# Kernel tuning notes

Hardware: AMD Instinct MI355X
Metric: run time of the kernel (lower is better)

Reference implementation:

```python
import jax, jax.numpy as jnp
import numpy as np

N, E, H, G, T = 10000, 160000, 256, 64, 1


def _lin(k, cin, cout):
    return jax.random.normal(k, (cin, cout), jnp.float32) * np.float32(1.0 / np.sqrt(cin))


def setup_inputs() -> dict:
    key = jax.random.key(0)
    ks = jax.random.split(key, 12)
    d = {}
    i = 0
    for p in ("lp", "pk", "lg"):
        d[p + "_node_feats"] = jax.random.normal(ks[i], (N, H), jnp.float32); i += 1
        d[p + "_edge_feats"] = jax.random.normal(ks[i], (E, H), jnp.float32); i += 1
        d[p + "_edge_index"] = jax.random.randint(ks[i], (2, E), 0, N); i += 1
        d[p + "_batch"] = jnp.sort(jax.random.randint(ks[i], (N,), 0, G)); i += 1
    wk = jax.random.split(jax.random.fold_in(key, 1), 6)
    d["W1"] = _lin(wk[0], H, H); d["b1"] = jnp.zeros((H,), jnp.float32)
    d["W2"] = _lin(wk[1], H, H); d["b2"] = jnp.zeros((H,), jnp.float32)
    d["W3"] = _lin(wk[2], H, H); d["b3"] = jnp.zeros((H,), jnp.float32)
    d["V1"] = _lin(wk[3], 2 * H, H); d["c1"] = jnp.zeros((H,), jnp.float32)
    d["V2"] = _lin(wk[4], H, H); d["c2"] = jnp.zeros((H,), jnp.float32)
    d["V3"] = _lin(wk[5], H, T); d["c3"] = jnp.zeros((T,), jnp.float32)
    d["num_graphs"] = G
    return d


def _mlp1(x, W1, b1, W2, b2, W3, b3):
    # make_mlp(c_in=H, c_hidden=H, c_out=H, num_layers=2), SiLU activations,
    # mlp_output_activation=SiLU
    h = jax.nn.silu(x @ W1 + b1)
    h = jax.nn.silu(h @ W2 + b2)
    return jax.nn.silu(h @ W3 + b3)


def _mlp2(x, V1, c1, V2, c2, V3, c3):
    # make_mlp(c_in=2H, c_hidden=H, c_out=num_tasks), output_activation=None
    h = jax.nn.silu(x @ V1 + c1)
    h = jax.nn.silu(h @ V2 + c2)
    return h @ V3 + c3


def _head(nf, ef, eidx, batch, num_graphs, p1, p2):
    n = nf.shape[0]
    # nodes branch: MLP then scatter-sum to graph level
    pooled_n = jax.ops.segment_sum(_mlp1(nf, *p1), batch, num_segments=num_graphs)
    # edges branch: MLP, scatter-sum edges->receiver nodes, then nodes->graphs
    pe = jax.ops.segment_sum(_mlp1(ef, *p1), eidx[1], num_segments=n)
    pooled_e = jax.ops.segment_sum(pe, batch, num_segments=num_graphs)
    return _mlp2(jnp.concatenate([pooled_n, pooled_e], axis=-1), *p2)


def reference(lp_node_feats, lp_edge_feats, lp_edge_index, lp_batch,
              pk_node_feats, pk_edge_feats, pk_edge_index, pk_batch,
              lg_node_feats, lg_edge_feats, lg_edge_index, lg_batch,
              num_graphs, W1, b1, W2, b2, W3, b3, V1, c1, V2, c2, V3, c3):
    p1 = (W1, b1, W2, b2, W3, b3)
    p2 = (V1, c1, V2, c2, V3, c3)
    out_lp = _head(lp_node_feats, lp_edge_feats, lp_edge_index, lp_batch, num_graphs, p1, p2)
    out_pk = _head(pk_node_feats, pk_edge_feats, pk_edge_index, pk_batch, num_graphs, p1, p2)
    out_lg = _head(lg_node_feats, lg_edge_feats, lg_edge_index, lg_batch, num_graphs, p1, p2)
    # output = pooled['ligand_pocket'] - pooled['pocket'] - pooled['ligand']
    return out_lp - out_pk - out_lg
```

## Files before the change

kernel.cpp:

```cpp
#include <hip/hip_runtime.h>
#include <hip/hip_bf16.h>

#define HD 256
#define NG 64
#define NNODES 10000
#define NEDGES 160000
#define MBLK 256
#define NTHREADS 512

typedef __attribute__((ext_vector_type(8))) short short8;
typedef __attribute__((ext_vector_type(4))) float f32x4;

__device__ __forceinline__ unsigned short f2bf(float f) {
  unsigned int u = __float_as_uint(f);
  u += 0x7FFFu + ((u >> 16) & 1u);
  return (unsigned short)(u >> 16);
}
__device__ __forceinline__ float silu_f(float x) {
  return x / (1.0f + __expf(-x));
}

__global__ void prep_weights(const float* __restrict__ W1, const float* __restrict__ W2,
                             const float* __restrict__ W3, unsigned short* __restrict__ Wt) {
  int idx = blockIdx.x * blockDim.x + threadIdx.x;
  int mat = idx >> 16;
  int rem = idx & 65535;
  int n = rem >> 8, k = rem & 255;
  const float* W = (mat == 0) ? W1 : (mat == 1) ? W2 : W3;
  Wt[idx] = f2bf(W[k * 256 + n]);
}

__global__ __launch_bounds__(NTHREADS, 2)
void fused_mlp1_pool(
    const float* __restrict__ nf0, const float* __restrict__ ef0,
    const int* __restrict__ ei0, const int* __restrict__ bt0,
    const float* __restrict__ nf1, const float* __restrict__ ef1,
    const int* __restrict__ ei1, const int* __restrict__ bt1,
    const float* __restrict__ nf2, const float* __restrict__ ef2,
    const int* __restrict__ ei2, const int* __restrict__ bt2,
    const float* __restrict__ b1, const float* __restrict__ b2,
    const float* __restrict__ b3,
    const unsigned short* __restrict__ Wt, float* __restrict__ pooled) {

  extern __shared__ char lds_raw[];
  char* stageB = lds_raw;
  char* SB = lds_raw + 131072;

  const int tid = threadIdx.x;
  const int wid = tid >> 6, lane = tid & 63;
  const int l15 = lane & 15, lhi = lane >> 4;
  const int wr = wid >> 2, wc = wid & 3;

  const int bid = blockIdx.x;
  const int head = bid / 85;
  const int r85 = bid % 85;
  const int isEdge = (r85 >= 5) ? 1 : 0;
  const int lb = isEdge ? (r85 - 5) : r85;
  const int Bs = isEdge ? 80 : 5;
  const int rows = isEdge ? NEDGES : NNODES;
  const int ntiles = (rows + MBLK - 1) / MBLK;

  const float* X; const int* bt; const int* recv;
  if (head == 0)      { X = isEdge ? ef0 : nf0; bt = bt0; recv = ei0 + NEDGES; }
  else if (head == 1) { X = isEdge ? ef1 : nf1; bt = bt1; recv = ei1 + NEDGES; }
  else                { X = isEdge ? ef2 : nf2; bt = bt2; recv = ei2 + NEDGES; }
  float* pool = pooled + (head * 2 + isEdge) * (NG * HD);

  f32x4 pacc[4][2];
  #pragma unroll
  for (int mt = 0; mt < 4; mt++)
    #pragma unroll
    for (int n = 0; n < 2; n++) pacc[mt][n] = (f32x4){0.f, 0.f, 0.f, 0.f};

  #pragma unroll
  for (int i = 0; i < 4; i++) ((int4*)SB)[tid + NTHREADS * i] = make_int4(0, 0, 0, 0);
  __syncthreads();

  for (int t = lb; t < ntiles; t += Bs) {
    const int rbase = t * MBLK;

    #pragma unroll 4
    for (int i = 0; i < 32; i++) {
      int rr = wid + i * 8;
      int gr = rbase + rr; if (gr > rows - 1) gr = rows - 1;
      f32x4 v = *(const f32x4*)(X + (long)gr * HD + lane * 4);
      unsigned long long pk =
          (unsigned long long)f2bf(v.x) |
          ((unsigned long long)f2bf(v.y) << 16) |
          ((unsigned long long)f2bf(v.z) << 32) |
          ((unsigned long long)f2bf(v.w) << 48);
      int byte = (rr * 512 + lane * 8) ^ ((rr & 7) << 4);
      *(unsigned long long*)(stageB + byte) = pk;
    }
    if (tid < MBLK) {
      int gr = rbase + tid;
      if (gr < rows) {
        int g = isEdge ? bt[recv[gr]] : bt[gr];
        int byte = (g * 512 + tid * 2) ^ ((g & 7) << 4);
        *(unsigned short*)(SB + byte) = 0x3F80;
      }
    }
    __syncthreads();

    #pragma unroll 1
    for (int layer = 0; layer < 3; layer++) {
      const unsigned short* Wl = Wt + layer * 65536;
      const float* bias = (layer == 0) ? b1 : (layer == 1) ? b2 : b3;

      f32x4 acc[8][4];
      #pragma unroll
      for (int n = 0; n < 4; n++) {
        float bv = bias[wc * 64 + n * 16 + l15];
        #pragma unroll
        for (int m = 0; m < 8; m++) acc[m][n] = (f32x4){bv, bv, bv, bv};
      }

      #pragma unroll 2
      for (int k = 0; k < 8; k++) {
        short8 bfrag[4];
        #pragma unroll
        for (int n = 0; n < 4; n++) {
          int cout = wc * 64 + n * 16 + l15;
          bfrag[n] = *(const short8*)(Wl + cout * 256 + k * 32 + lhi * 8);
        }
        #pragma unroll
        for (int m = 0; m < 8; m++) {
          int row = wr * 128 + m * 16 + l15;
          int byte = (row * 512 + k * 64 + lhi * 16) ^ ((row & 7) << 4);
          short8 a = *(const short8*)(stageB + byte);
          #pragma unroll
          for (int n = 0; n < 4; n++)
            acc[m][n] = __builtin_amdgcn_mfma_f32_16x16x32_bf16(a, bfrag[n], acc[m][n], 0, 0, 0);
        }
      }
      __syncthreads();

      if (layer < 2) {
        #pragma unroll
        for (int m = 0; m < 8; m++) {
          #pragma unroll
          for (int n = 0; n < 4; n++) {
            int col = wc * 64 + n * 16 + l15;
            #pragma unroll
            for (int j = 0; j < 4; j++) {
              int row = wr * 128 + m * 16 + lhi * 4 + j;
              unsigned short hv = f2bf(silu_f(acc[m][n][j]));
              int byte = (row * 512 + col * 2) ^ ((row & 7) << 4);
              *(unsigned short*)(stageB + byte) = hv;
            }
          }
        }
      } else {
        #pragma unroll
        for (int m = 0; m < 8; m++) {
          #pragma unroll
          for (int n = 0; n < 4; n++) {
            int col = wc * 64 + n * 16 + l15;
            int row0 = wr * 128 + m * 16 + lhi * 4;
            unsigned long long pk =
                (unsigned long long)f2bf(silu_f(acc[m][n][0])) |
                ((unsigned long long)f2bf(silu_f(acc[m][n][1])) << 16) |
                ((unsigned long long)f2bf(silu_f(acc[m][n][2])) << 32) |
                ((unsigned long long)f2bf(silu_f(acc[m][n][3])) << 48);
            int byte = (col * 512 + row0 * 2) ^ ((col & 7) << 4);
            *(unsigned long long*)(stageB + byte) = pk;
          }
        }
      }
      __syncthreads();
    }

    #pragma unroll 2
    for (int k = 0; k < 8; k++) {
      short8 bh[2];
      #pragma unroll
      for (int n = 0; n < 2; n++) {
        int col = wid * 32 + n * 16 + l15;
        int byte = (col * 512 + k * 64 + lhi * 16) ^ ((col & 7) << 4);
        bh[n] = *(const short8*)(stageB + byte);
      }
      #pragma unroll
      for (int mt = 0; mt < 4; mt++) {
        int g = mt * 16 + l15;
        int byte = (g * 512 + k * 64 + lhi * 16) ^ ((g & 7) << 4);
        short8 aS = *(const short8*)(SB + byte);
        #pragma unroll
        for (int n = 0; n < 2; n++)
          pacc[mt][n] = __builtin_amdgcn_mfma_f32_16x16x32_bf16(aS, bh[n], pacc[mt][n], 0, 0, 0);
      }
    }
    __syncthreads();
    #pragma unroll
    for (int i = 0; i < 4; i++) ((int4*)SB)[tid + NTHREADS * i] = make_int4(0, 0, 0, 0);
    __syncthreads();
  }

  #pragma unroll
  for (int mt = 0; mt < 4; mt++) {
    #pragma unroll
    for (int n = 0; n < 2; n++) {
      int col = wid * 32 + n * 16 + l15;
      #pragma unroll
      for (int j = 0; j < 4; j++) {
        int g = mt * 16 + lhi * 4 + j;
        unsafeAtomicAdd(&pool[g * HD + col], pacc[mt][n][j]);
      }
    }
  }
}

__global__ void mlp2_kernel(const float* __restrict__ pooled,
                            const float* __restrict__ V1, const float* __restrict__ c1,
                            const float* __restrict__ V2, const float* __restrict__ c2,
                            const float* __restrict__ V3, const float* __restrict__ c3,
                            float* __restrict__ out) {
  __shared__ float x[512];
  __shared__ float hb[256];
  __shared__ float wsum[4];
  const int g = blockIdx.x, t = threadIdx.x;
  float total = 0.0f;

  #pragma unroll 1
  for (int head = 0; head < 3; head++) {
    x[t]       = pooled[(head * 2 + 0) * NG * HD + g * HD + t];
    x[t + 256] = pooled[(head * 2 + 1) * NG * HD + g * HD + t];
    __syncthreads();

    float a = c1[t];
    #pragma unroll 8
    for (int k = 0; k < 512; k++) a += x[k] * V1[k * HD + t];
    a = silu_f(a);
    hb[t] = a;
    __syncthreads();

    float b = c2[t];
    #pragma unroll 8
    for (int k = 0; k < 256; k++) b += hb[k] * V2[k * HD + t];
    b = silu_f(b);

    float p = b * V3[t];
    #pragma unroll
    for (int off = 32; off > 0; off >>= 1) p += __shfl_down(p, off, 64);
    if ((t & 63) == 0) wsum[t >> 6] = p;
    __syncthreads();
    if (t == 0) {
      float s = wsum[0] + wsum[1] + wsum[2] + wsum[3] + c3[0];
      total += (head == 0) ? s : -s;
    }
    __syncthreads();
  }
  if (t == 0) out[g] = total;
}

extern "C" void kernel_launch(void* const* d_in, const int* in_sizes, int n_in,
                              void* d_out, int out_size, void* d_ws, size_t ws_size,
                              hipStream_t stream) {
  const float* nf0 = (const float*)d_in[0];
  const float* ef0 = (const float*)d_in[1];
  const int*   ei0 = (const int*)d_in[2];
  const int*   bt0 = (const int*)d_in[3];
  const float* nf1 = (const float*)d_in[4];
  const float* ef1 = (const float*)d_in[5];
  const int*   ei1 = (const int*)d_in[6];
  const int*   bt1 = (const int*)d_in[7];
  const float* nf2 = (const float*)d_in[8];
  const float* ef2 = (const float*)d_in[9];
  const int*   ei2 = (const int*)d_in[10];
  const int*   bt2 = (const int*)d_in[11];
  const float* W1 = (const float*)d_in[12]; const float* b1 = (const float*)d_in[13];
  const float* W2 = (const float*)d_in[14]; const float* b2 = (const float*)d_in[15];
  const float* W3 = (const float*)d_in[16]; const float* b3 = (const float*)d_in[17];
  const float* V1 = (const float*)d_in[18]; const float* c1 = (const float*)d_in[19];
  const float* V2 = (const float*)d_in[20]; const float* c2 = (const float*)d_in[21];
  const float* V3 = (const float*)d_in[22]; const float* c3 = (const float*)d_in[23];

  float* pooled = (float*)d_ws;
  unsigned short* Wt = (unsigned short*)((char*)d_ws + 393216);

  hipMemsetAsync(pooled, 0, 393216, stream);
  prep_weights<<<768, 256, 0, stream>>>(W1, W2, W3, Wt);

  hipFuncSetAttribute((const void*)fused_mlp1_pool,
                      hipFuncAttributeMaxDynamicSharedMemorySize, 163840);
  fused_mlp1_pool<<<255, NTHREADS, 163840, stream>>>(
      nf0, ef0, ei0, bt0, nf1, ef1, ei1, bt1, nf2, ef2, ei2, bt2,
      b1, b2, b3, Wt, pooled);

  mlp2_kernel<<<64, 256, 0, stream>>>(pooled, V1, c1, V2, c2, V3, c3, (float*)d_out);
}
```

Measured before the change: 1.373 ms.

## Use 1024-thread blocks, transposed MFMA epilogue with packed bf16 stores, split mlp2 per head

```diff
diff --git a/kernel.cpp b/kernel.cpp
--- a/kernel.cpp
+++ b/kernel.cpp
@@ -6,18 +6,18 @@
 #define NNODES 10000
 #define NEDGES 160000
 #define MBLK 256
-#define NTHREADS 512
+#define NTHREADS 1024
 
 typedef __attribute__((ext_vector_type(8))) short short8;
 typedef __attribute__((ext_vector_type(4))) float f32x4;
 
-__device__ __forceinline__ unsigned short f2bf(float f) {
-  unsigned int u = __float_as_uint(f);
-  u += 0x7FFFu + ((u >> 16) & 1u);
-  return (unsigned short)(u >> 16);
+__device__ __forceinline__ unsigned int pkbf2(float a, float b) {
+  __hip_bfloat162 h = __float22bfloat162_rn(float2{a, b});
+  return *reinterpret_cast<unsigned int*>(&h);
 }
 __device__ __forceinline__ float silu_f(float x) {
-  return x / (1.0f + __expf(-x));
+  float e = __builtin_amdgcn_exp2f(-1.442695041f * x);
+  return x * __builtin_amdgcn_rcpf(1.0f + e);
 }
 
 __global__ void prep_weights(const float* __restrict__ W1, const float* __restrict__ W2,
@@ -27,10 +27,11 @@
   int rem = idx & 65535;
   int n = rem >> 8, k = rem & 255;
   const float* W = (mat == 0) ? W1 : (mat == 1) ? W2 : W3;
-  Wt[idx] = f2bf(W[k * 256 + n]);
-}
-
-__global__ __launch_bounds__(NTHREADS, 2)
+  __hip_bfloat16 h = __float2bfloat16(W[k * 256 + n]);
+  Wt[idx] = *reinterpret_cast<unsigned short*>(&h);
+}
+
+__global__ __launch_bounds__(NTHREADS)
 void fused_mlp1_pool(
     const float* __restrict__ nf0, const float* __restrict__ ef0,
     const int* __restrict__ ei0, const int* __restrict__ bt0,
@@ -50,6 +51,7 @@
   const int wid = tid >> 6, lane = tid & 63;
   const int l15 = lane & 15, lhi = lane >> 4;
   const int wr = wid >> 2, wc = wid & 3;
+  const int wrow = wr * 64, wcol = wc * 64;
 
   const int bid = blockIdx.x;
   const int head = bid / 85;
@@ -66,31 +68,25 @@
   else                { X = isEdge ? ef2 : nf2; bt = bt2; recv = ei2 + NEDGES; }
   float* pool = pooled + (head * 2 + isEdge) * (NG * HD);
 
-  f32x4 pacc[4][2];
-  #pragma unroll
-  for (int mt = 0; mt < 4; mt++)
-    #pragma unroll
-    for (int n = 0; n < 2; n++) pacc[mt][n] = (f32x4){0.f, 0.f, 0.f, 0.f};
-
-  #pragma unroll
-  for (int i = 0; i < 4; i++) ((int4*)SB)[tid + NTHREADS * i] = make_int4(0, 0, 0, 0);
+  f32x4 pacc[4];
+  #pragma unroll
+  for (int mt = 0; mt < 4; mt++) pacc[mt] = (f32x4){0.f, 0.f, 0.f, 0.f};
+
+  #pragma unroll
+  for (int i = 0; i < 2; i++) ((int4*)SB)[tid + NTHREADS * i] = make_int4(0, 0, 0, 0);
   __syncthreads();
 
   for (int t = lb; t < ntiles; t += Bs) {
     const int rbase = t * MBLK;
 
     #pragma unroll 4
-    for (int i = 0; i < 32; i++) {
-      int rr = wid + i * 8;
+    for (int i = 0; i < 16; i++) {
+      int rr = wid + i * 16;
       int gr = rbase + rr; if (gr > rows - 1) gr = rows - 1;
       f32x4 v = *(const f32x4*)(X + (long)gr * HD + lane * 4);
-      unsigned long long pk =
-          (unsigned long long)f2bf(v.x) |
-          ((unsigned long long)f2bf(v.y) << 16) |
-          ((unsigned long long)f2bf(v.z) << 32) |
-          ((unsigned long long)f2bf(v.w) << 48);
+      uint2 pk = make_uint2(pkbf2(v.x, v.y), pkbf2(v.z, v.w));
       int byte = (rr * 512 + lane * 8) ^ ((rr & 7) << 4);
-      *(unsigned long long*)(stageB + byte) = pk;
+      *(uint2*)(stageB + byte) = pk;
     }
     if (tid < MBLK) {
       int gr = rbase + tid;
@@ -107,63 +103,73 @@
       const unsigned short* Wl = Wt + layer * 65536;
       const float* bias = (layer == 0) ? b1 : (layer == 1) ? b2 : b3;
 
-      f32x4 acc[8][4];
-      #pragma unroll
-      for (int n = 0; n < 4; n++) {
-        float bv = bias[wc * 64 + n * 16 + l15];
-        #pragma unroll
-        for (int m = 0; m < 8; m++) acc[m][n] = (f32x4){bv, bv, bv, bv};
+      f32x4 acc[4][4];
+      if (layer < 2) {
+        #pragma unroll
+        for (int ct = 0; ct < 4; ct++) {
+          f32x4 bv = *(const f32x4*)(bias + wcol + ct * 16 + lhi * 4);
+          #pragma unroll
+          for (int rt = 0; rt < 4; rt++) acc[rt][ct] = bv;
+        }
+      } else {
+        #pragma unroll
+        for (int ct = 0; ct < 4; ct++) {
+          float bv = bias[wcol + ct * 16 + l15];
+          #pragma unroll
+          for (int rt = 0; rt < 4; rt++) acc[rt][ct] = (f32x4){bv, bv, bv, bv};
+        }
       }
 
       #pragma unroll 2
       for (int k = 0; k < 8; k++) {
-        short8 bfrag[4];
-        #pragma unroll
-        for (int n = 0; n < 4; n++) {
-          int cout = wc * 64 + n * 16 + l15;
-          bfrag[n] = *(const short8*)(Wl + cout * 256 + k * 32 + lhi * 8);
-        }
-        #pragma unroll
-        for (int m = 0; m < 8; m++) {
-          int row = wr * 128 + m * 16 + l15;
+        short8 wfrag[4];
+        #pragma unroll
+        for (int ct = 0; ct < 4; ct++)
+          wfrag[ct] = *(const short8*)(Wl + (wcol + ct * 16 + l15) * 256 + k * 32 + lhi * 8);
+        #pragma unroll
+        for (int rt = 0; rt < 4; rt++) {
+          int row = wrow + rt * 16 + l15;
           int byte = (row * 512 + k * 64 + lhi * 16) ^ ((row & 7) << 4);
-          short8 a = *(const short8*)(stageB + byte);
-          #pragma unroll
-          for (int n = 0; n < 4; n++)
-            acc[m][n] = __builtin_amdgcn_mfma_f32_16x16x32_bf16(a, bfrag[n], acc[m][n], 0, 0, 0);
+          short8 xf = *(const short8*)(stageB + byte);
+          if (layer < 2) {
+            #pragma unroll
+            for (int ct = 0; ct < 4; ct++)
+              acc[rt][ct] = __builtin_amdgcn_mfma_f32_16x16x32_bf16(wfrag[ct], xf, acc[rt][ct], 0, 0, 0);
+          } else {
+            #pragma unroll
+            for (int ct = 0; ct < 4; ct++)
+              acc[rt][ct] = __builtin_amdgcn_mfma_f32_16x16x32_bf16(xf, wfrag[ct], acc[rt][ct], 0, 0, 0);
+          }
         }
       }
       __syncthreads();
 
       if (layer < 2) {
         #pragma unroll
-        for (int m = 0; m < 8; m++) {
-          #pragma unroll
-          for (int n = 0; n < 4; n++) {
-            int col = wc * 64 + n * 16 + l15;
-            #pragma unroll
-            for (int j = 0; j < 4; j++) {
-              int row = wr * 128 + m * 16 + lhi * 4 + j;
-              unsigned short hv = f2bf(silu_f(acc[m][n][j]));
-              int byte = (row * 512 + col * 2) ^ ((row & 7) << 4);
-              *(unsigned short*)(stageB + byte) = hv;
-            }
+        for (int rt = 0; rt < 4; rt++) {
+          int row = wrow + rt * 16 + l15;
+          #pragma unroll
+          for (int ct = 0; ct < 4; ct++) {
+            int c0 = wcol + ct * 16 + lhi * 4;
+            f32x4 a = acc[rt][ct];
+            uint2 pk = make_uint2(pkbf2(silu_f(a.x), silu_f(a.y)),
+                                  pkbf2(silu_f(a.z), silu_f(a.w)));
+            int byte = (row * 512 + c0 * 2) ^ ((row & 7) << 4);
+            *(uint2*)(stageB + byte) = pk;
           }
         }
       } else {
         #pragma unroll
-        for (int m = 0; m < 8; m++) {
-          #pragma unroll
-          for (int n = 0; n < 4; n++) {
-            int col = wc * 64 + n * 16 + l15;
-            int row0 = wr * 128 + m * 16 + lhi * 4;
-            unsigned long long pk =
-                (unsigned long long)f2bf(silu_f(acc[m][n][0])) |
-                ((unsigned long long)f2bf(silu_f(acc[m][n][1])) << 16) |
-                ((unsigned long long)f2bf(silu_f(acc[m][n][2])) << 32) |
-                ((unsigned long long)f2bf(silu_f(acc[m][n][3])) << 48);
+        for (int rt = 0; rt < 4; rt++) {
+          int row0 = wrow + rt * 16 + lhi * 4;
+          #pragma unroll
+          for (int ct = 0; ct < 4; ct++) {
+            int col = wcol + ct * 16 + l15;
+            f32x4 a = acc[rt][ct];
+            uint2 pk = make_uint2(pkbf2(silu_f(a.x), silu_f(a.y)),
+                                  pkbf2(silu_f(a.z), silu_f(a.w)));
             int byte = (col * 512 + row0 * 2) ^ ((col & 7) << 4);
-            *(unsigned long long*)(stageB + byte) = pk;
+            *(uint2*)(stageB + byte) = pk;
           }
         }
       }
@@ -172,39 +178,30 @@
 
     #pragma unroll 2
     for (int k = 0; k < 8; k++) {
-      short8 bh[2];
-      #pragma unroll
-      for (int n = 0; n < 2; n++) {
-        int col = wid * 32 + n * 16 + l15;
-        int byte = (col * 512 + k * 64 + lhi * 16) ^ ((col & 7) << 4);
-        bh[n] = *(const short8*)(stageB + byte);
-      }
+      int col = wid * 16 + l15;
+      int byteB = (col * 512 + k * 64 + lhi * 16) ^ ((col & 7) << 4);
+      short8 bh = *(const short8*)(stageB + byteB);
       #pragma unroll
       for (int mt = 0; mt < 4; mt++) {
         int g = mt * 16 + l15;
-        int byte = (g * 512 + k * 64 + lhi * 16) ^ ((g & 7) << 4);
-        short8 aS = *(const short8*)(SB + byte);
-        #pragma unroll
-        for (int n = 0; n < 2; n++)
-          pacc[mt][n] = __builtin_amdgcn_mfma_f32_16x16x32_bf16(aS, bh[n], pacc[mt][n], 0, 0, 0);
+        int byteA = (g * 512 + k * 64 + lhi * 16) ^ ((g & 7) << 4);
+        short8 aS = *(const short8*)(SB + byteA);
+        pacc[mt] = __builtin_amdgcn_mfma_f32_16x16x32_bf16(aS, bh, pacc[mt], 0, 0, 0);
       }
     }
     __syncthreads();
     #pragma unroll
-    for (int i = 0; i < 4; i++) ((int4*)SB)[tid + NTHREADS * i] = make_int4(0, 0, 0, 0);
+    for (int i = 0; i < 2; i++) ((int4*)SB)[tid + NTHREADS * i] = make_int4(0, 0, 0, 0);
     __syncthreads();
   }
 
   #pragma unroll
   for (int mt = 0; mt < 4; mt++) {
+    int col = wid * 16 + l15;
     #pragma unroll
-    for (int n = 0; n < 2; n++) {
-      int col = wid * 32 + n * 16 + l15;
-      #pragma unroll
-      for (int j = 0; j < 4; j++) {
-        int g = mt * 16 + lhi * 4 + j;
-        unsafeAtomicAdd(&pool[g * HD + col], pacc[mt][n][j]);
-      }
+    for (int j = 0; j < 4; j++) {
+      int g = mt * 16 + lhi * 4 + j;
+      unsafeAtomicAdd(&pool[g * HD + col], pacc[mt][j]);
     }
   }
 }
@@ -217,39 +214,33 @@
   __shared__ float x[512];
   __shared__ float hb[256];
   __shared__ float wsum[4];
-  const int g = blockIdx.x, t = threadIdx.x;
-  float total = 0.0f;
-
-  #pragma unroll 1
-  for (int head = 0; head < 3; head++) {
-    x[t]       = pooled[(head * 2 + 0) * NG * HD + g * HD + t];
-    x[t + 256] = pooled[(head * 2 + 1) * NG * HD + g * HD + t];
-    __syncthreads();
-
-    float a = c1[t];
-    #pragma unroll 8
-    for (int k = 0; k < 512; k++) a += x[k] * V1[k * HD + t];
-    a = silu_f(a);
-    hb[t] = a;
-    __syncthreads();
-
-    float b = c2[t];
-    #pragma unroll 8
-    for (int k = 0; k < 256; k++) b += hb[k] * V2[k * HD + t];
-    b = silu_f(b);
-
-    float p = b * V3[t];
-    #pragma unroll
-    for (int off = 32; off > 0; off >>= 1) p += __shfl_down(p, off, 64);
-    if ((t & 63) == 0) wsum[t >> 6] = p;
-    __syncthreads();
-    if (t == 0) {
-      float s = wsum[0] + wsum[1] + wsum[2] + wsum[3] + c3[0];
-      total += (head == 0) ? s : -s;
-    }
-    __syncthreads();
+  const int g = blockIdx.x & 63, head = blockIdx.x >> 6, t = threadIdx.x;
+
+  x[t]       = pooled[(head * 2 + 0) * NG * HD + g * HD + t];
+  x[t + 256] = pooled[(head * 2 + 1) * NG * HD + g * HD + t];
+  __syncthreads();
+
+  float a = c1[t];
+  #pragma unroll 8
+  for (int k = 0; k < 512; k++) a += x[k] * V1[k * HD + t];
+  a = silu_f(a);
+  hb[t] = a;
+  __syncthreads();
+
+  float b = c2[t];
+  #pragma unroll 8
+  for (int k = 0; k < 256; k++) b += hb[k] * V2[k * HD + t];
+  b = silu_f(b);
+
+  float p = b * V3[t];
+  #pragma unroll
+  for (int off = 32; off > 0; off >>= 1) p += __shfl_down(p, off, 64);
+  if ((t & 63) == 0) wsum[t >> 6] = p;
+  __syncthreads();
+  if (t == 0) {
+    float s = wsum[0] + wsum[1] + wsum[2] + wsum[3] + c3[0];
+    unsafeAtomicAdd(&out[g], (head == 0) ? s : -s);
   }
-  if (t == 0) out[g] = total;
 }
 
 extern "C" void kernel_launch(void* const* d_in, const int* in_sizes, int n_in,
@@ -278,6 +269,7 @@
   unsigned short* Wt = (unsigned short*)((char*)d_ws + 393216);
 
   hipMemsetAsync(pooled, 0, 393216, stream);
+  hipMemsetAsync(d_out, 0, out_size * sizeof(float), stream);
   prep_weights<<<768, 256, 0, stream>>>(W1, W2, W3, Wt);
 
   hipFuncSetAttribute((const void*)fused_mlp1_pool,
@@ -286,5 +278,5 @@
       nf0, ef0, ei0, bt0, nf1, ef1, ei1, bt1, nf2, ef2, ei2, bt2,
       b1, b2, b3, Wt, pooled);
 
-  mlp2_kernel<<<64, 256, 0, stream>>>(pooled, V1, c1, V2, c2, V3, c3, (float*)d_out);
-}
+  mlp2_kernel<<<192, 256, 0, stream>>>(pooled, V1, c1, V2, c2, V3, c3, (float*)d_out);
+}
```

New measurement: 1.510 ms. 1.1x slower.
